# Optimization experiments

Hardware: AMD Instinct MI355X
Metric: run time of the kernel (lower is better)

The kernel has to match this reference:

```python
import jax, jax.numpy as jnp
import numpy as np

B, T, N, D_IN = 2, 64, 64, 512
HID, L, H = 256, 2, 4
C = HID // H  # 64 per-head channels
NEG_SLOPE = 0.2
LN_EPS = 1e-5


def setup_inputs() -> dict:
    key = jax.random.key(0)
    ks = jax.random.split(key, 8)
    s_in = 1.0 / np.sqrt(D_IN)
    s_h = 1.0 / np.sqrt(HID)
    s_c = 1.0 / np.sqrt(C)
    return {
        "x": jax.random.normal(ks[0], (B, T, N, D_IN), jnp.float32),
        "person_mask": jax.random.randint(ks[1], (B, T, N), 0, 2) > 0,
        "W_in": (jax.random.normal(ks[2], (D_IN, HID)) * s_in).astype(jnp.float32),
        "b_in": jnp.zeros((HID,), jnp.float32),
        "Wl": (jax.random.normal(ks[3], (L, HID, HID)) * s_h).astype(jnp.float32),
        "bl": jnp.zeros((L, HID), jnp.float32),
        "Wr": (jax.random.normal(ks[4], (L, HID, HID)) * s_h).astype(jnp.float32),
        "br": jnp.zeros((L, HID), jnp.float32),
        "att": (jax.random.normal(ks[5], (L, H, C)) * s_c).astype(jnp.float32),
        "out_bias": jnp.zeros((L, HID), jnp.float32),
        "ln_scale": jnp.ones((L, HID), jnp.float32),
        "ln_bias": jnp.zeros((L, HID), jnp.float32),
    }


def _layernorm(x, g, b):
    mu = jnp.mean(x, axis=-1, keepdims=True)
    var = jnp.mean(jnp.square(x - mu), axis=-1, keepdims=True)
    return (x - mu) * jax.lax.rsqrt(var + LN_EPS) * g + b


def _gatv2_layer(h, allowed, Wl, bl, Wr, br, att, ob):
    # h: [bt, N, HID]; allowed: [bt, N, N] bool (edge j->i at [b,i,j])
    bt, n, _ = h.shape
    xl = (h @ Wl + bl).reshape(bt, n, H, C)  # source features (messages)
    xr = (h @ Wr + br).reshape(bt, n, H, C)  # target features
    # GATv2 logit: e_ij = a . leaky_relu(xr_i + xl_j), per head
    s = xr[:, :, None, :, :] + xl[:, None, :, :, :]  # [bt, i, j, H, C]
    e = jnp.einsum('bijhc,hc->bijh', jax.nn.leaky_relu(s, NEG_SLOPE), att)
    e = jnp.where(allowed[..., None], e, -1e9)
    alpha = jax.nn.softmax(e, axis=2)  # segment softmax over incoming edges j
    out = jnp.einsum('bijh,bjhc->bihc', alpha, xl)  # weighted scatter-sum
    return out.reshape(bt, n, H * C) + ob


def _forward(x, person_mask, W_in, b_in, Wl, bl, Wr, br, att, out_bias, ln_scale, ln_bias):
    b, t, n, _ = x.shape
    bt = b * t
    h = (x @ W_in + b_in).reshape(bt, n, HID)
    m = person_mask.reshape(bt, n)
    # edges: all pairs among masked nodes (incl. diag) + self loops for every node
    allowed = (m[:, :, None] & m[:, None, :]) | jnp.eye(n, dtype=bool)[None]
    hi = h
    for li in range(L):
        res = hi
        g = _gatv2_layer(hi, allowed, Wl[li], bl[li], Wr[li], br[li], att[li], out_bias[li])
        g = jax.nn.elu(g)  # dropout is identity in eval mode
        g = _layernorm(g, ln_scale[li], ln_bias[li])
        hi = g + res  # use_residual=True
        hi = jnp.where(m[:, :, None], hi, 0.0)
    # graphs with <=1 masked node are skipped (pass through projected features)
    keep = (jnp.sum(m, axis=-1) > 1)[:, None, None]
    out = jnp.where(keep, hi, h)
    return out.reshape(b, t, n, HID)


def reference(x, person_mask, W_in, b_in, Wl, bl, Wr, br, att, out_bias, ln_scale, ln_bias):
    return _forward(x, person_mask, W_in, b_in, Wl, bl, Wr, br, att, out_bias, ln_scale, ln_bias)
```

## Files before the change

### kernel.cpp

```cpp
#include <hip/hip_runtime.h>
#include <hip/hip_bf16.h>

#define BT_G   128
#define NND    64
#define D_IN_  512
#define HID_   256
#define NH     4
#define NCH    64
#define NROWS  8192
#define LN_EPS_    1e-5f

typedef __hip_bfloat16 bf16;
typedef __attribute__((ext_vector_type(8))) short short8;
typedef __attribute__((ext_vector_type(4))) float float4v;

__device__ __forceinline__ float toF(bf16 x) { return __bfloat162float(x); }

__global__ __launch_bounds__(256) void transpose_all_kernel(
    const float* __restrict__ W_in, const float* __restrict__ Wl,
    const float* __restrict__ Wr, const unsigned int* __restrict__ mw,
    bf16* __restrict__ WTin, bf16* __restrict__ WlrT, int* __restrict__ mout) {
    const int z = blockIdx.z;
    const int tid = threadIdx.x;
    if (z == 5) {
        if (blockIdx.x || blockIdx.y) return;
        __shared__ int okInt, okF32, okB16, okByte;
        if (tid == 0) { okInt = 1; okF32 = 1; okB16 = 1; okByte = 1; }
        __syncthreads();
        int aI = 1, aF = 1, aB = 1, aC = 1;
        for (int i = tid; i < 2048; i += 256) {
            unsigned w = mw[i];
            aI &= (w <= 1u);
            aF &= (w == 0u || w == 0x3F800000u);
            unsigned lo = w & 0xFFFFu, hi = w >> 16;
            aB &= ((lo == 0u || lo == 0x3F80u) && (hi == 0u || hi == 0x3F80u));
            aC &= (((w | (w >> 8) | (w >> 16) | (w >> 24)) & 0xFEu) == 0u);
        }
        if (!aI) atomicAnd(&okInt, 0);
        if (!aF) atomicAnd(&okF32, 0);
        if (!aB) atomicAnd(&okB16, 0);
        if (!aC) atomicAnd(&okByte, 0);
        __syncthreads();
        const int layout = (okInt || okF32) ? 0 : (okB16 ? 2 : (okByte ? 3 : 0));
        for (int i = tid; i < NROWS; i += 256) {
            int v;
            if (layout == 2)      v = (((const unsigned short*)mw)[i] != 0);
            else if (layout == 3) v = (((const unsigned char*)mw)[i] != 0);
            else                  v = (mw[i] != 0u);
            mout[i] = v;
        }
        return;
    }
    __shared__ float t[32][33];
    const float* src; bf16* dst; int K;
    if (z == 0)      { src = W_in;                 dst = WTin;                    K = 512; }
    else if (z <= 2) { src = Wl + (z - 1) * 65536; dst = WlrT + (z - 1) * 131072; K = 256; }
    else             { src = Wr + (z - 3) * 65536; dst = WlrT + (z - 3) * 131072 + 256 * 256; K = 256; }
    const int n0 = blockIdx.x * 32, k0 = blockIdx.y * 32;
    if (k0 >= K) return;
    const int tx = tid & 31, ty = tid >> 5;
    #pragma unroll
    for (int i = 0; i < 4; ++i)
        t[ty + 8 * i][tx] = src[(size_t)(k0 + ty + 8 * i) * 256 + n0 + tx];
    __syncthreads();
    #pragma unroll
    for (int i = 0; i < 4; ++i)
        dst[(size_t)(n0 + ty + 8 * i) * K + k0 + tx] =
            __float2bfloat16(t[tx][ty + 8 * i]);
}

__global__ __launch_bounds__(256) void gemm_in_kernel(
    const float* __restrict__ A, const bf16* __restrict__ BT,
    const float* __restrict__ bias, float* __restrict__ Cf,
    bf16* __restrict__ Cb16)
{
    __shared__ bf16 As[64 * 72];
    __shared__ bf16 Bs[64 * 72];
    const int tid  = threadIdx.x;
    const int wave = tid >> 6, lane = tid & 63;
    const int quad = lane >> 4, l16 = lane & 15;
    const int m0 = blockIdx.y * 64, n0 = blockIdx.x * 64;
    const int wm = (wave & 1) * 32, wn = (wave >> 1) * 32;
    float4v acc[2][2] = {};
    const int r  = tid >> 2;
    const int cq = (tid & 3) * 16;

    for (int k0 = 0; k0 < D_IN_; k0 += 64) {
        const float* sa = A + (size_t)(m0 + r) * D_IN_ + k0 + cq;
        const float4 f0 = *(const float4*)(sa);
        const float4 f1 = *(const float4*)(sa + 4);
        const float4 f2 = *(const float4*)(sa + 8);
        const float4 f3 = *(const float4*)(sa + 12);
        const bf16* sb = BT + (size_t)(n0 + r) * D_IN_ + k0 + cq;
        const float4 b0 = *(const float4*)(sb);
        const float4 b1 = *(const float4*)(sb + 8);
        union { bf16 h[16]; float4 v[2]; } u;
        u.h[0]=__float2bfloat16(f0.x); u.h[1]=__float2bfloat16(f0.y);
        u.h[2]=__float2bfloat16(f0.z); u.h[3]=__float2bfloat16(f0.w);
        u.h[4]=__float2bfloat16(f1.x); u.h[5]=__float2bfloat16(f1.y);
        u.h[6]=__float2bfloat16(f1.z); u.h[7]=__float2bfloat16(f1.w);
        u.h[8]=__float2bfloat16(f2.x); u.h[9]=__float2bfloat16(f2.y);
        u.h[10]=__float2bfloat16(f2.z); u.h[11]=__float2bfloat16(f2.w);
        u.h[12]=__float2bfloat16(f3.x); u.h[13]=__float2bfloat16(f3.y);
        u.h[14]=__float2bfloat16(f3.z); u.h[15]=__float2bfloat16(f3.w);
        __syncthreads();
        *(float4*)(&As[r * 72 + cq])     = u.v[0];
        *(float4*)(&As[r * 72 + cq + 8]) = u.v[1];
        *(float4*)(&Bs[r * 72 + cq])     = b0;
        *(float4*)(&Bs[r * 72 + cq + 8]) = b1;
        __syncthreads();
        #pragma unroll
        for (int kk = 0; kk < 64; kk += 32) {
            short8 af[2], bf2[2];
            #pragma unroll
            for (int mi = 0; mi < 2; ++mi)
                af[mi] = *(const short8*)(&As[(wm + mi * 16 + l16) * 72 + kk + quad * 8]);
            #pragma unroll
            for (int ni = 0; ni < 2; ++ni)
                bf2[ni] = *(const short8*)(&Bs[(wn + ni * 16 + l16) * 72 + kk + quad * 8]);
            #pragma unroll
            for (int mi = 0; mi < 2; ++mi)
                #pragma unroll
                for (int ni = 0; ni < 2; ++ni)
                    acc[mi][ni] = __builtin_amdgcn_mfma_f32_16x16x32_bf16(
                        af[mi], bf2[ni], acc[mi][ni], 0, 0, 0);
        }
    }
    #pragma unroll
    for (int ni = 0; ni < 2; ++ni) {
        const int col = n0 + wn + ni * 16 + l16;
        const float bv = bias[col];
        #pragma unroll
        for (int mi = 0; mi < 2; ++mi)
            #pragma unroll
            for (int rr = 0; rr < 4; ++rr) {
                const int row = m0 + wm + mi * 16 + quad * 4 + rr;
                const float v = acc[mi][ni][rr] + bv;
                Cf[(size_t)row * HID_ + col] = v;
                Cb16[(size_t)row * HID_ + col] = __float2bfloat16(v);
            }
    }
}

__global__ __launch_bounds__(256) void gemm_mfma_kernel(
    const bf16* __restrict__ A, const bf16* __restrict__ BT,
    const float* __restrict__ bias0, const float* __restrict__ bias1,
    float* __restrict__ Ca, float* __restrict__ Cbf, int M, int K)
{
    __shared__ bf16 As[128 * 72];
    __shared__ bf16 Bs[64 * 72];
    const int tid  = threadIdx.x;
    const int wave = tid >> 6, lane = tid & 63;
    const int quad = lane >> 4, l16 = lane & 15;
    const int m0 = blockIdx.y * 128, n0g = blockIdx.x * 64;
    const int wm = (wave & 1) * 64, wn = (wave >> 1) * 32;
    float4v acc[4][2] = {};
    const int r  = tid >> 2;
    const int cq = (tid & 3) * 16;

    for (int k0 = 0; k0 < K; k0 += 64) {
        const bf16* sa0 = A  + (size_t)(m0 + r) * K + k0 + cq;
        const bf16* sa1 = sa0 + (size_t)64 * K;
        const bf16* sb  = BT + (size_t)(n0g + r) * K + k0 + cq;
        const float4 a00 = *(const float4*)(sa0);
        const float4 a01 = *(const float4*)(sa0 + 8);
        const float4 a10 = *(const float4*)(sa1);
        const float4 a11 = *(const float4*)(sa1 + 8);
        const float4 b0  = *(const float4*)(sb);
        const float4 b1  = *(const float4*)(sb + 8);
        __syncthreads();
        *(float4*)(&As[r * 72 + cq])            = a00;
        *(float4*)(&As[r * 72 + cq + 8])        = a01;
        *(float4*)(&As[(r + 64) * 72 + cq])     = a10;
        *(float4*)(&As[(r + 64) * 72 + cq + 8]) = a11;
        *(float4*)(&Bs[r * 72 + cq])            = b0;
        *(float4*)(&Bs[r * 72 + cq + 8])        = b1;
        __syncthreads();
        #pragma unroll
        for (int kk = 0; kk < 64; kk += 32) {
            short8 af[4], bf2[2];
            #pragma unroll
            for (int mi = 0; mi < 4; ++mi)
                af[mi] = *(const short8*)(&As[(wm + mi * 16 + l16) * 72 + kk + quad * 8]);
            #pragma unroll
            for (int ni = 0; ni < 2; ++ni)
                bf2[ni] = *(const short8*)(&Bs[(wn + ni * 16 + l16) * 72 + kk + quad * 8]);
            #pragma unroll
            for (int mi = 0; mi < 4; ++mi)
                #pragma unroll
                for (int ni = 0; ni < 2; ++ni)
                    acc[mi][ni] = __builtin_amdgcn_mfma_f32_16x16x32_bf16(
                        af[mi], bf2[ni], acc[mi][ni], 0, 0, 0);
        }
    }
    const bool loHalf = (n0g < 256);
    float* Co = loHalf ? Ca : Cbf;
    const float* bp = loHalf ? bias0 : bias1;
    const int cbase = loHalf ? n0g : (n0g - 256);
    #pragma unroll
    for (int ni = 0; ni < 2; ++ni) {
        const int col = cbase + wn + ni * 16 + l16;
        const float bv = bp[col];
        #pragma unroll
        for (int mi = 0; mi < 4; ++mi)
            #pragma unroll
            for (int rr = 0; rr < 4; ++rr) {
                const int row = m0 + wm + mi * 16 + quad * 4 + rr;
                Co[(size_t)row * 256 + col] = acc[mi][ni][rr] + bv;
            }
    }
}

__global__ __launch_bounds__(256) void attn_kernel(
    const float* xl, const float* xr, const float* att,
    const int* msk, float* g)
{
    __shared__ float xls [64][68];
    __shared__ float xlsT[64][68];
    __shared__ float xrsT[64][36];
    __shared__ float av[64], P[32], Q[64], mxf[32], inv[32];
    __shared__ float pmax[8][32], psum[8][32];
    __shared__ int   ms[64];
    float (*esT)[36] = (float(*)[36])xlsT;

    const int tid   = threadIdx.x;
    const int head  = blockIdx.x >> 1;
    const int half  = blockIdx.x & 1;
    const int gr    = blockIdx.y;
    const int ibase = half * 32;
    const int ti = tid >> 4, tj = tid & 15;
    const int i0 = ti * 2, j0 = tj * 4;

    const float* xlg = xl + (size_t)gr * NND * HID_ + head * NCH;
    const float* xrg = xr + ((size_t)gr * NND + ibase) * HID_ + head * NCH;

    {
        const int r  = tid >> 2;
        const int c0 = (tid & 3) * 16;
        const int r2 = tid >> 3;
        const int cb = (tid & 7) * 8;
        float a[4][4], b[2][4];
        #pragma unroll
        for (int k = 0; k < 4; ++k)
            *(float4*)a[k] = *(const float4*)(xlg + r * HID_ + c0 + 4 * k);
        *(float4*)b[0] = *(const float4*)(xrg + r2 * HID_ + cb);
        *(float4*)b[1] = *(const float4*)(xrg + r2 * HID_ + cb + 4);
        #pragma unroll
        for (int k = 0; k < 4; ++k)
            *(float4*)&xls[r][c0 + 4 * k] = *(float4*)a[k];
        #pragma unroll
        for (int k = 0; k < 4; ++k)
            #pragma unroll
            for (int w = 0; w < 4; ++w)
                xlsT[c0 + 4 * k + w][r] = a[k][w];
        #pragma unroll
        for (int k = 0; k < 2; ++k)
            #pragma unroll
            for (int w = 0; w < 4; ++w)
                xrsT[cb + 4 * k + w][r2] = b[k][w];
        if (tid < 64) {
            av[tid] = att[head * NCH + tid];
            ms[tid] = msk[gr * NND + tid];
        }
    }
    __syncthreads();

    float aa[2][4] = {};
    for (int c = 0; c < 64; ++c) {
        const float a = av[c];
        const float2 xr2 = *(const float2*)&xrsT[c][i0];
        const float4 xl4 = *(const float4*)&xlsT[c][j0];
        const float xrv[2] = {xr2.x, xr2.y};
        const float xlv[4] = {xl4.x, xl4.y, xl4.z, xl4.w};
        #pragma unroll
        for (int y = 0; y < 2; ++y)
            #pragma unroll
            for (int x = 0; x < 4; ++x)
                aa[y][x] = fmaf(a, fabsf(xrv[y] + xlv[x]), aa[y][x]);
    }
    if (tid < 32) {
        float s = 0.f;
        for (int c = 0; c < 64; ++c) s = fmaf(av[c], xrsT[c][tid], s);
        P[tid] = s;
    } else if (tid >= 64 && tid < 128) {
        const int j = tid - 64;
        float s = 0.f;
        for (int c = 0; c < 64; ++c) s = fmaf(av[c], xlsT[c][j], s);
        Q[j] = s;
    }
    __syncthreads();

    {
        float Pv[2], Qv[4]; int mi2[2], mj4[4];
        #pragma unroll
        for (int y = 0; y < 2; ++y) { Pv[y] = P[i0 + y]; mi2[y] = ms[ibase + i0 + y]; }
        #pragma unroll
        for (int x = 0; x < 4; ++x) { Qv[x] = Q[j0 + x]; mj4[x] = ms[j0 + x]; }
        #pragma unroll
        for (int x = 0; x < 4; ++x) {
            float col[2];
            #pragma unroll
            for (int y = 0; y < 2; ++y) {
                float e = fmaf(0.4f, aa[y][x], 0.6f * (Pv[y] + Qv[x]));
                const bool allowed = (mi2[y] && mj4[x]) || (ibase + i0 + y == j0 + x);
                col[y] = allowed ? e : -1e9f;
            }
            *(float2*)&esT[j0 + x][i0] = *(float2*)col;
        }
    }
    __syncthreads();

    {
        const int si = tid & 31, q = tid >> 5;
        float mx = -1e30f;
        #pragma unroll
        for (int k = 0; k < 8; ++k) mx = fmaxf(mx, esT[8 * q + k][si]);
        pmax[q][si] = mx;
    }
    __syncthreads();
    if (tid < 32) {
        float m = pmax[0][tid];
        #pragma unroll
        for (int q = 1; q < 8; ++q) m = fmaxf(m, pmax[q][tid]);
        mxf[tid] = m;
    }
    __syncthreads();
    {
        const int si = tid & 31, q = tid >> 5;
        const float mx = mxf[si];
        float s = 0.f;
        #pragma unroll
        for (int k = 0; k < 8; ++k) {
            const float ev = __expf(esT[8 * q + k][si] - mx);
            esT[8 * q + k][si] = ev;
            s += ev;
        }
        psum[q][si] = s;
    }
    __syncthreads();
    if (tid < 32) {
        float s = psum[0][tid];
        #pragma unroll
        for (int q = 1; q < 8; ++q) s += psum[q][tid];
        inv[tid] = 1.f / s;
    }
    __syncthreads();

    {
        float oa[2][4] = {};
        for (int j = 0; j < 64; ++j) {
            const float2 al = *(const float2*)&esT[j][i0];
            const float4 xv = *(const float4*)&xls[j][j0];
            const float alv[2] = {al.x, al.y};
            const float xvv[4] = {xv.x, xv.y, xv.z, xv.w};
            #pragma unroll
            for (int y = 0; y < 2; ++y)
                #pragma unroll
                for (int x = 0; x < 4; ++x)
                    oa[y][x] = fmaf(alv[y], xvv[x], oa[y][x]);
        }
        #pragma unroll
        for (int y = 0; y < 2; ++y) {
            const float iv = inv[i0 + y];
            float o[4];
            #pragma unroll
            for (int x = 0; x < 4; ++x) o[x] = oa[y][x] * iv;
            float* go = g + (size_t)(gr * NND + ibase + i0 + y) * HID_ + head * NCH + j0;
            *(float4*)go = *(float4*)o;
        }
    }
}

__global__ __launch_bounds__(256) void epilogue_kernel(
    const float* __restrict__ g, const float* res,
    const float* __restrict__ ob, const float* __restrict__ lns,
    const float* __restrict__ lnb, const int* __restrict__ msk,
    float* hout, bf16* hb, int finalSel)
{
    const int lane = threadIdx.x & 63;
    const int wave = threadIdx.x >> 6;
    const int m = blockIdx.x * 4 + wave;
    if (finalSel) {
        const int gr = m >> 6;
        const int mv = msk[gr * NND + lane];
        const unsigned long long bal = __ballot(mv != 0);
        if (__popcll(bal) <= 1) return;
    }
    const float* grow = g + (size_t)m * HID_;
    float v[4];
    float sum = 0.f;
    #pragma unroll
    for (int q = 0; q < 4; ++q) {
        const int c = q * 64 + lane;
        float x = grow[c] + ob[c];
        x = x > 0.f ? x : (__expf(x) - 1.f);
        v[q] = x; sum += x;
    }
    #pragma unroll
    for (int off = 1; off < 64; off <<= 1) sum += __shfl_xor(sum, off);
    const float mu = sum * (1.f / 256.f);
    float vs = 0.f;
    #pragma unroll
    for (int q = 0; q < 4; ++q) { const float d = v[q] - mu; vs += d * d; }
    #pragma unroll
    for (int off = 1; off < 64; off <<= 1) vs += __shfl_xor(vs, off);
    const float rstd = rsqrtf(vs * (1.f / 256.f) + LN_EPS_);
    const int mnode = msk[m];
    const float* rrow = res + (size_t)m * HID_;
    float* ho = hout + (size_t)m * HID_;
    #pragma unroll
    for (int q = 0; q < 4; ++q) {
        const int c = q * 64 + lane;
        float y = (v[q] - mu) * rstd * lns[c] + lnb[c];
        y += rrow[c];
        y = mnode ? y : 0.f;
        ho[c] = y;
        if (hb) hb[(size_t)m * HID_ + c] = __float2bfloat16(y);
    }
}

extern "C" void kernel_launch(void* const* d_in, const int* in_sizes, int n_in,
                              void* d_out, int out_size, void* d_ws, size_t ws_size,
                              hipStream_t stream) {
    const float* x    = (const float*)d_in[0];
    const float* W_in = (const float*)d_in[2];
    const float* b_in = (const float*)d_in[3];
    const float* Wl   = (const float*)d_in[4];
    const float* bl   = (const float*)d_in[5];
    const float* Wr   = (const float*)d_in[6];
    const float* br   = (const float*)d_in[7];
    const float* att  = (const float*)d_in[8];
    const float* ob   = (const float*)d_in[9];
    const float* lns  = (const float*)d_in[10];
    const float* lnb  = (const float*)d_in[11];
    float* out = (float*)d_out;

    char* w = (char*)d_ws;
    int*   mcan = (int*)w;                      w += 32768;
    float* h    = (float*)w;                    w += (size_t)NROWS * HID_ * 4;
    float* xlb  = (float*)w;                    w += (size_t)NROWS * HID_ * 4;
    float* xrb  = (float*)w;                    w += (size_t)NROWS * HID_ * 4;
    bf16*  hxb  = (bf16*)w;                     w += (size_t)NROWS * HID_ * 2;
    bf16*  WTin = (bf16*)w;                     w += (size_t)D_IN_ * HID_ * 2;
    bf16*  WlrT = (bf16*)w;
    float* gb   = xrb;

    transpose_all_kernel<<<dim3(8, 16, 6), 256, 0, stream>>>(
        W_in, Wl, Wr, (const unsigned int*)d_in[1], WTin, WlrT, mcan);

    gemm_in_kernel<<<dim3(HID_ / 64, NROWS / 64), 256, 0, stream>>>(
        x, WTin, b_in, out, hxb);

    for (int li = 0; li < 2; ++li) {
        const float* resf = (li == 0) ? out : h;
        gemm_mfma_kernel<<<dim3(512 / 64, NROWS / 128), 256, 0, stream>>>(
            hxb, WlrT + (size_t)li * 512 * HID_, bl + li * HID_, br + li * HID_,
            xlb, xrb, NROWS, HID_);
        attn_kernel<<<dim3(NH * 2, BT_G), 256, 0, stream>>>(
            xlb, xrb, att + li * NH * NCH, mcan, gb);
        if (li == 0) {
            epilogue_kernel<<<NROWS / 4, 256, 0, stream>>>(
                gb, resf, ob, lns, lnb, mcan, h, hxb, 0);
        } else {
            epilogue_kernel<<<NROWS / 4, 256, 0, stream>>>(
                gb, resf, ob + HID_, lns + HID_, lnb + HID_, mcan,
                out, (bf16*)nullptr, 1);
        }
    }

    (void)in_sizes; (void)n_in; (void)out_size; (void)ws_size;
}
```

Measured before the change: 178.9 us.

## Fuse weight prep into input GEMM and layer-0 epilogue into layer-1 projection GEMM

Merges the weight transpose, mask canonicalisation and input projection GEMM into one launch; the input GEMM now transposes W_in in shared memory itself instead of reading a pre-transposed copy. The layer-0 ELU/LayerNorm/residual/mask epilogue is folded into the prologue of the layer-1 Wl/Wr GEMM, so the normalized activations go straight to shared memory as bf16. This removes two launches and a round trip of the intermediate through global memory. In exchange, the epilogue work is repeated by each of the 8 column blocks, LDS use rises to about 76KB per block, and the transposed Bs store is strided.

```diff
diff --git a/kernel.cpp b/kernel.cpp
--- a/kernel.cpp
+++ b/kernel.cpp
@@ -14,34 +14,128 @@
 typedef __attribute__((ext_vector_type(8))) short short8;
 typedef __attribute__((ext_vector_type(4))) float float4v;
 
-__device__ __forceinline__ float toF(bf16 x) { return __bfloat162float(x); }
-
-__global__ __launch_bounds__(256) void transpose_all_kernel(
-    const float* __restrict__ W_in, const float* __restrict__ Wl,
-    const float* __restrict__ Wr, const unsigned int* __restrict__ mw,
-    bf16* __restrict__ WTin, bf16* __restrict__ WlrT, int* __restrict__ mout) {
-    const int z = blockIdx.z;
+union PrepArena {
+    float t[32][33];
+    struct { bf16 As[64 * 72]; bf16 Bs[64 * 72]; } g;
+    int flags[4];
+};
+
+__global__ __launch_bounds__(256) void prep_gemm_in_kernel(
+    const float* __restrict__ x, const unsigned* __restrict__ mw,
+    const float* __restrict__ W_in, const float* __restrict__ b_in,
+    const float* __restrict__ Wl, const float* __restrict__ Wr,
+    float* __restrict__ Cf, bf16* __restrict__ Cb16,
+    bf16* __restrict__ WlrT, int* __restrict__ mout)
+{
+    __shared__ PrepArena ar;
     const int tid = threadIdx.x;
-    if (z == 5) {
-        if (blockIdx.x || blockIdx.y) return;
-        __shared__ int okInt, okF32, okB16, okByte;
-        if (tid == 0) { okInt = 1; okF32 = 1; okB16 = 1; okByte = 1; }
+    const int bid = blockIdx.x;
+
+    if (bid < 512) {
+        bf16* As = ar.g.As;
+        bf16* Bs = ar.g.Bs;
+        const int wave = tid >> 6, lane = tid & 63;
+        const int quad = lane >> 4, l16 = lane & 15;
+        const int m0 = (bid >> 2) * 64, n0 = (bid & 3) * 64;
+        const int wm = (wave & 1) * 32, wn = (wave >> 1) * 32;
+        float4v acc[2][2] = {};
+        const int r  = tid >> 2;
+        const int cq = (tid & 3) * 16;
+        for (int k0 = 0; k0 < D_IN_; k0 += 64) {
+            const float* sa = x + (size_t)(m0 + r) * D_IN_ + k0 + cq;
+            const float4 f0 = *(const float4*)(sa);
+            const float4 f1 = *(const float4*)(sa + 4);
+            const float4 f2 = *(const float4*)(sa + 8);
+            const float4 f3 = *(const float4*)(sa + 12);
+            const float* sw = W_in + (size_t)(k0 + r) * HID_ + n0 + cq;
+            float wv[16];
+            *(float4*)(wv)      = *(const float4*)(sw);
+            *(float4*)(wv + 4)  = *(const float4*)(sw + 4);
+            *(float4*)(wv + 8)  = *(const float4*)(sw + 8);
+            *(float4*)(wv + 12) = *(const float4*)(sw + 12);
+            union { bf16 hh[16]; float4 v[2]; } u;
+            u.hh[0]=__float2bfloat16(f0.x); u.hh[1]=__float2bfloat16(f0.y);
+            u.hh[2]=__float2bfloat16(f0.z); u.hh[3]=__float2bfloat16(f0.w);
+            u.hh[4]=__float2bfloat16(f1.x); u.hh[5]=__float2bfloat16(f1.y);
+            u.hh[6]=__float2bfloat16(f1.z); u.hh[7]=__float2bfloat16(f1.w);
+            u.hh[8]=__float2bfloat16(f2.x); u.hh[9]=__float2bfloat16(f2.y);
+            u.hh[10]=__float2bfloat16(f2.z); u.hh[11]=__float2bfloat16(f2.w);
+            u.hh[12]=__float2bfloat16(f3.x); u.hh[13]=__float2bfloat16(f3.y);
+            u.hh[14]=__float2bfloat16(f3.z); u.hh[15]=__float2bfloat16(f3.w);
+            __syncthreads();
+            *(float4*)(&As[r * 72 + cq])     = u.v[0];
+            *(float4*)(&As[r * 72 + cq + 8]) = u.v[1];
+            #pragma unroll
+            for (int j = 0; j < 16; ++j)
+                Bs[(cq + j) * 72 + r] = __float2bfloat16(wv[j]);
+            __syncthreads();
+            #pragma unroll
+            for (int kk = 0; kk < 64; kk += 32) {
+                short8 af[2], bf2[2];
+                #pragma unroll
+                for (int mi = 0; mi < 2; ++mi)
+                    af[mi] = *(const short8*)(&As[(wm + mi * 16 + l16) * 72 + kk + quad * 8]);
+                #pragma unroll
+                for (int ni = 0; ni < 2; ++ni)
+                    bf2[ni] = *(const short8*)(&Bs[(wn + ni * 16 + l16) * 72 + kk + quad * 8]);
+                #pragma unroll
+                for (int mi = 0; mi < 2; ++mi)
+                    #pragma unroll
+                    for (int ni = 0; ni < 2; ++ni)
+                        acc[mi][ni] = __builtin_amdgcn_mfma_f32_16x16x32_bf16(
+                            af[mi], bf2[ni], acc[mi][ni], 0, 0, 0);
+            }
+        }
+        #pragma unroll
+        for (int ni = 0; ni < 2; ++ni) {
+            const int col = n0 + wn + ni * 16 + l16;
+            const float bv = b_in[col];
+            #pragma unroll
+            for (int mi = 0; mi < 2; ++mi)
+                #pragma unroll
+                for (int rr = 0; rr < 4; ++rr) {
+                    const int row = m0 + wm + mi * 16 + quad * 4 + rr;
+                    const float v = acc[mi][ni][rr] + bv;
+                    Cf[(size_t)row * HID_ + col] = v;
+                    Cb16[(size_t)row * HID_ + col] = __float2bfloat16(v);
+                }
+        }
+    } else if (bid < 768) {
+        const int q = bid - 512;
+        const int z4 = q >> 6;
+        const int s = q & 63;
+        const int n0 = (s & 7) * 32, k0 = (s >> 3) * 32;
+        const float* src = (z4 < 2) ? (Wl + z4 * 65536) : (Wr + (z4 - 2) * 65536);
+        bf16* dst = WlrT + ((z4 < 2) ? (size_t)z4 * 131072
+                                     : (size_t)(z4 - 2) * 131072 + 65536);
+        const int tx = tid & 31, ty = tid >> 5;
+        #pragma unroll
+        for (int i = 0; i < 4; ++i)
+            ar.t[ty + 8 * i][tx] = src[(size_t)(k0 + ty + 8 * i) * 256 + n0 + tx];
+        __syncthreads();
+        #pragma unroll
+        for (int i = 0; i < 4; ++i)
+            dst[(size_t)(n0 + ty + 8 * i) * 256 + k0 + tx] =
+                __float2bfloat16(ar.t[tx][ty + 8 * i]);
+    } else {
+        int* fl = ar.flags;
+        if (tid == 0) { fl[0] = 1; fl[1] = 1; fl[2] = 1; fl[3] = 1; }
         __syncthreads();
         int aI = 1, aF = 1, aB = 1, aC = 1;
         for (int i = tid; i < 2048; i += 256) {
-            unsigned w = mw[i];
-            aI &= (w <= 1u);
-            aF &= (w == 0u || w == 0x3F800000u);
-            unsigned lo = w & 0xFFFFu, hi = w >> 16;
+            const unsigned w2 = mw[i];
+            aI &= (w2 <= 1u);
+            aF &= (w2 == 0u || w2 == 0x3F800000u);
+            const unsigned lo = w2 & 0xFFFFu, hi = w2 >> 16;
             aB &= ((lo == 0u || lo == 0x3F80u) && (hi == 0u || hi == 0x3F80u));
-            aC &= (((w | (w >> 8) | (w >> 16) | (w >> 24)) & 0xFEu) == 0u);
-        }
-        if (!aI) atomicAnd(&okInt, 0);
-        if (!aF) atomicAnd(&okF32, 0);
-        if (!aB) atomicAnd(&okB16, 0);
-        if (!aC) atomicAnd(&okByte, 0);
-        __syncthreads();
-        const int layout = (okInt || okF32) ? 0 : (okB16 ? 2 : (okByte ? 3 : 0));
+            aC &= (((w2 | (w2 >> 8) | (w2 >> 16) | (w2 >> 24)) & 0xFEu) == 0u);
+        }
+        if (!aI) atomicAnd(&fl[0], 0);
+        if (!aF) atomicAnd(&fl[1], 0);
+        if (!aB) atomicAnd(&fl[2], 0);
+        if (!aC) atomicAnd(&fl[3], 0);
+        __syncthreads();
+        const int layout = (fl[0] || fl[1]) ? 0 : (fl[2] ? 2 : (fl[3] ? 3 : 0));
         for (int i = tid; i < NROWS; i += 256) {
             int v;
             if (layout == 2)      v = (((const unsigned short*)mw)[i] != 0);
@@ -49,96 +143,6 @@
             else                  v = (mw[i] != 0u);
             mout[i] = v;
         }
-        return;
-    }
-    __shared__ float t[32][33];
-    const float* src; bf16* dst; int K;
-    if (z == 0)      { src = W_in;                 dst = WTin;                    K = 512; }
-    else if (z <= 2) { src = Wl + (z - 1) * 65536; dst = WlrT + (z - 1) * 131072; K = 256; }
-    else             { src = Wr + (z - 3) * 65536; dst = WlrT + (z - 3) * 131072 + 256 * 256; K = 256; }
-    const int n0 = blockIdx.x * 32, k0 = blockIdx.y * 32;
-    if (k0 >= K) return;
-    const int tx = tid & 31, ty = tid >> 5;
-    #pragma unroll
-    for (int i = 0; i < 4; ++i)
-        t[ty + 8 * i][tx] = src[(size_t)(k0 + ty + 8 * i) * 256 + n0 + tx];
-    __syncthreads();
-    #pragma unroll
-    for (int i = 0; i < 4; ++i)
-        dst[(size_t)(n0 + ty + 8 * i) * K + k0 + tx] =
-            __float2bfloat16(t[tx][ty + 8 * i]);
-}
-
-__global__ __launch_bounds__(256) void gemm_in_kernel(
-    const float* __restrict__ A, const bf16* __restrict__ BT,
-    const float* __restrict__ bias, float* __restrict__ Cf,
-    bf16* __restrict__ Cb16)
-{
-    __shared__ bf16 As[64 * 72];
-    __shared__ bf16 Bs[64 * 72];
-    const int tid  = threadIdx.x;
-    const int wave = tid >> 6, lane = tid & 63;
-    const int quad = lane >> 4, l16 = lane & 15;
-    const int m0 = blockIdx.y * 64, n0 = blockIdx.x * 64;
-    const int wm = (wave & 1) * 32, wn = (wave >> 1) * 32;
-    float4v acc[2][2] = {};
-    const int r  = tid >> 2;
-    const int cq = (tid & 3) * 16;
-
-    for (int k0 = 0; k0 < D_IN_; k0 += 64) {
-        const float* sa = A + (size_t)(m0 + r) * D_IN_ + k0 + cq;
-        const float4 f0 = *(const float4*)(sa);
-        const float4 f1 = *(const float4*)(sa + 4);
-        const float4 f2 = *(const float4*)(sa + 8);
-        const float4 f3 = *(const float4*)(sa + 12);
-        const bf16* sb = BT + (size_t)(n0 + r) * D_IN_ + k0 + cq;
-        const float4 b0 = *(const float4*)(sb);
-        const float4 b1 = *(const float4*)(sb + 8);
-        union { bf16 h[16]; float4 v[2]; } u;
-        u.h[0]=__float2bfloat16(f0.x); u.h[1]=__float2bfloat16(f0.y);
-        u.h[2]=__float2bfloat16(f0.z); u.h[3]=__float2bfloat16(f0.w);
-        u.h[4]=__float2bfloat16(f1.x); u.h[5]=__float2bfloat16(f1.y);
-        u.h[6]=__float2bfloat16(f1.z); u.h[7]=__float2bfloat16(f1.w);
-        u.h[8]=__float2bfloat16(f2.x); u.h[9]=__float2bfloat16(f2.y);
-        u.h[10]=__float2bfloat16(f2.z); u.h[11]=__float2bfloat16(f2.w);
-        u.h[12]=__float2bfloat16(f3.x); u.h[13]=__float2bfloat16(f3.y);
-        u.h[14]=__float2bfloat16(f3.z); u.h[15]=__float2bfloat16(f3.w);
-        __syncthreads();
-        *(float4*)(&As[r * 72 + cq])     = u.v[0];
-        *(float4*)(&As[r * 72 + cq + 8]) = u.v[1];
-        *(float4*)(&Bs[r * 72 + cq])     = b0;
-        *(float4*)(&Bs[r * 72 + cq + 8]) = b1;
-        __syncthreads();
-        #pragma unroll
-        for (int kk = 0; kk < 64; kk += 32) {
-            short8 af[2], bf2[2];
-            #pragma unroll
-            for (int mi = 0; mi < 2; ++mi)
-                af[mi] = *(const short8*)(&As[(wm + mi * 16 + l16) * 72 + kk + quad * 8]);
-            #pragma unroll
-            for (int ni = 0; ni < 2; ++ni)
-                bf2[ni] = *(const short8*)(&Bs[(wn + ni * 16 + l16) * 72 + kk + quad * 8]);
-            #pragma unroll
-            for (int mi = 0; mi < 2; ++mi)
-                #pragma unroll
-                for (int ni = 0; ni < 2; ++ni)
-                    acc[mi][ni] = __builtin_amdgcn_mfma_f32_16x16x32_bf16(
-                        af[mi], bf2[ni], acc[mi][ni], 0, 0, 0);
-        }
-    }
-    #pragma unroll
-    for (int ni = 0; ni < 2; ++ni) {
-        const int col = n0 + wn + ni * 16 + l16;
-        const float bv = bias[col];
-        #pragma unroll
-        for (int mi = 0; mi < 2; ++mi)
-            #pragma unroll
-            for (int rr = 0; rr < 4; ++rr) {
-                const int row = m0 + wm + mi * 16 + quad * 4 + rr;
-                const float v = acc[mi][ni][rr] + bv;
-                Cf[(size_t)row * HID_ + col] = v;
-                Cb16[(size_t)row * HID_ + col] = __float2bfloat16(v);
-            }
     }
 }
 
@@ -211,6 +215,103 @@
     }
 }
 
+__global__ __launch_bounds__(256, 2) void gemm_ep_kernel(
+    const float* __restrict__ g0, const float* __restrict__ res,
+    const float* __restrict__ ob0, const float* __restrict__ lns0,
+    const float* __restrict__ lnb0, const int* __restrict__ msk,
+    const bf16* __restrict__ BT, const float* __restrict__ bias0,
+    const float* __restrict__ bias1, float* __restrict__ hres,
+    float* __restrict__ Ca, float* __restrict__ Cbf)
+{
+    __shared__ bf16 As[128 * 264];
+    __shared__ bf16 Bs[64 * 72];
+    const int tid  = threadIdx.x;
+    const int wave = tid >> 6, lane = tid & 63;
+    const int quad = lane >> 4, l16 = lane & 15;
+    const int m0 = blockIdx.y * 128, n0g = blockIdx.x * 64;
+    const int wm = (wave & 1) * 64, wn = (wave >> 1) * 32;
+
+    for (int rr = wave; rr < 128; rr += 4) {
+        const int m = m0 + rr;
+        const float* grow = g0 + (size_t)m * HID_;
+        float v[4];
+        float sum = 0.f;
+        #pragma unroll
+        for (int q = 0; q < 4; ++q) {
+            const int c = q * 64 + lane;
+            float xv = grow[c] + ob0[c];
+            xv = xv > 0.f ? xv : (__expf(xv) - 1.f);
+            v[q] = xv; sum += xv;
+        }
+        #pragma unroll
+        for (int off = 1; off < 64; off <<= 1) sum += __shfl_xor(sum, off);
+        const float mu = sum * (1.f / 256.f);
+        float vs = 0.f;
+        #pragma unroll
+        for (int q = 0; q < 4; ++q) { const float d = v[q] - mu; vs += d * d; }
+        #pragma unroll
+        for (int off = 1; off < 64; off <<= 1) vs += __shfl_xor(vs, off);
+        const float rstd = rsqrtf(vs * (1.f / 256.f) + LN_EPS_);
+        const int mnode = msk[m];
+        const float* rrow = res + (size_t)m * HID_;
+        #pragma unroll
+        for (int q = 0; q < 4; ++q) {
+            const int c = q * 64 + lane;
+            float y = (v[q] - mu) * rstd * lns0[c] + lnb0[c];
+            y += rrow[c];
+            y = mnode ? y : 0.f;
+            if (n0g == 0) hres[(size_t)m * HID_ + c] = y;
+            As[rr * 264 + c] = __float2bfloat16(y);
+        }
+    }
+    __syncthreads();
+
+    float4v acc[4][2] = {};
+    const int r  = tid >> 2;
+    const int cq = (tid & 3) * 16;
+    for (int k0 = 0; k0 < HID_; k0 += 64) {
+        const bf16* sb = BT + (size_t)(n0g + r) * HID_ + k0 + cq;
+        const float4 b0 = *(const float4*)(sb);
+        const float4 b1 = *(const float4*)(sb + 8);
+        __syncthreads();
+        *(float4*)(&Bs[r * 72 + cq])     = b0;
+        *(float4*)(&Bs[r * 72 + cq + 8]) = b1;
+        __syncthreads();
+        #pragma unroll
+        for (int kk = 0; kk < 64; kk += 32) {
+            short8 af[4], bf2[2];
+            #pragma unroll
+            for (int mi = 0; mi < 4; ++mi)
+                af[mi] = *(const short8*)(&As[(wm + mi * 16 + l16) * 264 + k0 + kk + quad * 8]);
+            #pragma unroll
+            for (int ni = 0; ni < 2; ++ni)
+                bf2[ni] = *(const short8*)(&Bs[(wn + ni * 16 + l16) * 72 + kk + quad * 8]);
+            #pragma unroll
+            for (int mi = 0; mi < 4; ++mi)
+                #pragma unroll
+                for (int ni = 0; ni < 2; ++ni)
+                    acc[mi][ni] = __builtin_amdgcn_mfma_f32_16x16x32_bf16(
+                        af[mi], bf2[ni], acc[mi][ni], 0, 0, 0);
+        }
+    }
+    const bool loHalf = (n0g < 256);
+    float* Co = loHalf ? Ca : Cbf;
+    const float* bp = loHalf ? bias0 : bias1;
+    const int cbase = loHalf ? n0g : (n0g - 256);
+    #pragma unroll
+    for (int ni = 0; ni < 2; ++ni) {
+        const int col = cbase + wn + ni * 16 + l16;
+        const float bv = bp[col];
+        #pragma unroll
+        for (int mi = 0; mi < 4; ++mi)
+            #pragma unroll
+            for (int rr = 0; rr < 4; ++rr) {
+                const int row = m0 + wm + mi * 16 + quad * 4 + rr;
+                Co[(size_t)row * 256 + col] = acc[mi][ni][rr] + bv;
+            }
+    }
+}
+
 __global__ __launch_bounds__(256) void attn_kernel(
     const float* xl, const float* xr, const float* att,
     const int* msk, float* g)
@@ -439,34 +540,30 @@
     int*   mcan = (int*)w;                      w += 32768;
     float* h    = (float*)w;                    w += (size_t)NROWS * HID_ * 4;
     float* xlb  = (float*)w;                    w += (size_t)NROWS * HID_ * 4;
-    float* xrb  = (float*)w;                    w += (size_t)NROWS * HID_ * 4;
+    float* xra  = (float*)w;                    w += (size_t)NROWS * HID_ * 4;
+    float* xrb2 = (float*)w;                    w += (size_t)NROWS * HID_ * 4;
     bf16*  hxb  = (bf16*)w;                     w += (size_t)NROWS * HID_ * 2;
-    bf16*  WTin = (bf16*)w;                     w += (size_t)D_IN_ * HID_ * 2;
     bf16*  WlrT = (bf16*)w;
-    float* gb   = xrb;
-
-    transpose_all_kernel<<<dim3(8, 16, 6), 256, 0, stream>>>(
-        W_in, Wl, Wr, (const unsigned int*)d_in[1], WTin, WlrT, mcan);
-
-    gemm_in_kernel<<<dim3(HID_ / 64, NROWS / 64), 256, 0, stream>>>(
-        x, WTin, b_in, out, hxb);
-
-    for (int li = 0; li < 2; ++li) {
-        const float* resf = (li == 0) ? out : h;
-        gemm_mfma_kernel<<<dim3(512 / 64, NROWS / 128), 256, 0, stream>>>(
-            hxb, WlrT + (size_t)li * 512 * HID_, bl + li * HID_, br + li * HID_,
-            xlb, xrb, NROWS, HID_);
-        attn_kernel<<<dim3(NH * 2, BT_G), 256, 0, stream>>>(
-            xlb, xrb, att + li * NH * NCH, mcan, gb);
-        if (li == 0) {
-            epilogue_kernel<<<NROWS / 4, 256, 0, stream>>>(
-                gb, resf, ob, lns, lnb, mcan, h, hxb, 0);
-        } else {
-            epilogue_kernel<<<NROWS / 4, 256, 0, stream>>>(
-                gb, resf, ob + HID_, lns + HID_, lnb + HID_, mcan,
-                out, (bf16*)nullptr, 1);
-        }
-    }
+
+    prep_gemm_in_kernel<<<769, 256, 0, stream>>>(
+        x, (const unsigned*)d_in[1], W_in, b_in, Wl, Wr, out, hxb, WlrT, mcan);
+
+    gemm_mfma_kernel<<<dim3(512 / 64, NROWS / 128), 256, 0, stream>>>(
+        hxb, WlrT, bl, br, xlb, xra, NROWS, HID_);
+
+    attn_kernel<<<dim3(NH * 2, BT_G), 256, 0, stream>>>(
+        xlb, xra, att, mcan, xra);
+
+    gemm_ep_kernel<<<dim3(512 / 64, NROWS / 128), 256, 0, stream>>>(
+        xra, out, ob, lns, lnb, mcan,
+        WlrT + (size_t)512 * HID_, bl + HID_, br + HID_, h, xlb, xrb2);
+
+    attn_kernel<<<dim3(NH * 2, BT_G), 256, 0, stream>>>(
+        xlb, xrb2, att + NH * NCH, mcan, xrb2);
+
+    epilogue_kernel<<<NROWS / 4, 256, 0, stream>>>(
+        xrb2, h, ob + HID_, lns + HID_, lnb + HID_, mcan,
+        out, (bf16*)nullptr, 1);
 
     (void)in_sizes; (void)n_in; (void)out_size; (void)ws_size;
 }
```

Result: slower. 218.1 us (+21.9%).
